# Performance work log

Hardware: AMD Instinct MI355X
Metric: run time of the kernel (lower is better)

The kernel has to match this reference:

```python
import jax, jax.numpy as jnp
import numpy as np

CLS_IDX = 2
DIS_THRESH = 1.0
WEIGHT = 1.0
BIG = 1e9  # sentinel distance for non-boundary lines


def setup_inputs() -> dict:
    key = jax.random.key(0)
    k1, k2, k3, k4 = jax.random.split(key, 4)
    B, T, N, P = 64, 12, 2000, 20
    return {
        "pred_abs": jax.random.normal(k1, (B, T, 2), dtype=jnp.float32),
        "gt_map_pts": jax.random.normal(k2, (B, N, 1, P, 2), dtype=jnp.float32),
        "gt_map_labels": jax.random.randint(k3, (B, N), 0, 4),
        "gt_ego_fut_masks": jax.random.uniform(k4, (B, T), dtype=jnp.float32),
    }


def reference(pred_abs, gt_map_pts, gt_map_labels, gt_ego_fut_masks):
    # pred_abs: [B,T,2]; gt_map_pts: [B,N,1,P,2]; gt_map_labels: [B,N]; masks: [B,T]
    pred_abs = pred_abs.astype(jnp.float32)
    lines = gt_map_pts[:, :, 0].astype(jnp.float32)       # [B,N,P,2]
    valid_line = gt_map_labels == CLS_IDX                  # [B,N]
    has_lines = jnp.any(valid_line, axis=1)                # [B]

    # --- per-timestep min distance to boundary points ---
    diff = pred_abs[:, :, None, None, :] - lines[:, None, :, :, :]   # [B,T,N,P,2]
    dist = jnp.linalg.norm(diff, axis=-1)                            # [B,T,N,P]
    dist = jnp.where(valid_line[:, None, :, None], dist, BIG)
    min_dist = jnp.min(dist, axis=(2, 3))                            # [B,T]
    loss_t = jax.nn.relu(DIS_THRESH - min_dist)                      # [B,T]

    # --- segment intersection: ego step vs boundary segments ---
    origin = jnp.zeros((pred_abs.shape[0], 1, 2), dtype=jnp.float32)
    traj_ext = jnp.concatenate([origin, pred_abs], axis=1)           # [B,T+1,2]
    s1 = traj_ext[:, :-1]                                            # [B,T,2] seg start
    e1 = traj_ext[:, 1:]                                             # [B,T,2] seg end
    bs = lines[:, :, :-1, :]                                         # [B,N,P-1,2]
    be = lines[:, :, 1:, :]                                          # [B,N,P-1,2]

    d1 = e1 - s1                                                     # [B,T,2]
    d2 = be - bs                                                     # [B,N,P-1,2]
    dx1 = d1[..., 0][:, :, None, None]; dy1 = d1[..., 1][:, :, None, None]  # [B,T,1,1]
    dx2 = d2[..., 0][:, None]; dy2 = d2[..., 1][:, None]                    # [B,1,N,P-1]
    det = dx1 * dy2 - dx2 * dy1                                      # [B,T,N,P-1]
    parallel = det == 0
    safe_det = jnp.where(parallel, 1.0, det)
    rel = bs[:, None] - s1[:, :, None, None, :]                      # [B,T,N,P-1,2]
    rx = rel[..., 0]; ry = rel[..., 1]
    t1 = (rx * dy2 - ry * dx2) / safe_det
    t2 = (rx * dy1 - ry * dx1) / safe_det
    intersect = (t1 >= 0) & (t1 <= 1) & (t2 >= 0) & (t2 <= 1) & (~parallel)
    intersect = intersect & valid_line[:, None, :, None]
    crossed = jnp.any(intersect, axis=(2, 3))                        # [B,T]

    # --- early-break semantics: once a valid timestep crosses, drop it and all later t ---
    valid_t = (gt_ego_fut_masks >= 0.5) & has_lines[:, None]          # [B,T]
    trigger = valid_t & crossed
    blocked = jnp.cumsum(trigger.astype(jnp.int32), axis=1) > 0       # inclusive
    include = valid_t & (~blocked)                                    # [B,T]

    total = jnp.sum(jnp.where(include, loss_t, 0.0))
    n_valid = jnp.sum(include.astype(jnp.float32))
    loss = jnp.where(n_valid == 0, 0.0,
                     total / jnp.maximum(n_valid, 1.0) * WEIGHT)
    return jnp.reshape(loss, (1,))


if __name__ == "__main__":
    out = reference(**setup_inputs())
    print(out)
```

## Files before the change

### kernel.cpp

```cpp
#include <hip/hip_runtime.h>

#define BB 64
#define TT 12
#define NL 2000
#define PP 20
#define CLS 2
#define BIGF 1.0e9f

#define LPB   128
#define NBLK  16
#define NSLOT NBLK

#define OFF_CM  (TT * NSLOT * BB)
#define OFF_CNT (TT * NSLOT * BB + NSLOT * BB)

__global__ __launch_bounds__(64) void gtmb_main(
    const float* __restrict__ pred,
    const float* __restrict__ pts,
    const int*   __restrict__ labels,
    unsigned int* __restrict__ ws) {
    const int b    = blockIdx.y;
    const int blk  = blockIdx.x;
    const int lane = threadIdx.x;

    __shared__ unsigned short sidx[LPB];

    const int base = blk * LPB;
    const int n0 = base + 2 * lane;
    int v0 = 0, v1 = 0;
    if (n0 < NL) {
        int2 lb = *reinterpret_cast<const int2*>(labels + b * NL + n0);
        v0 = (lb.x == CLS);
        v1 = (lb.y == CLS);
    }
    unsigned long long m0 = __ballot(v0);
    unsigned long long m1 = __ballot(v1);
    unsigned long long lt = (1ull << lane) - 1ull;
    const int c0  = __popcll(m0);
    const int cnt = c0 + __popcll(m1);
    if (v0) sidx[__popcll(m0 & lt)]      = (unsigned short)n0;
    if (v1) sidx[c0 + __popcll(m1 & lt)] = (unsigned short)(n0 + 1);
    __syncthreads();

    float ex[TT], ey[TT];
    const float* pb = pred + b * (TT * 2);
#pragma unroll
    for (int t = 0; t < TT; ++t) { ex[t] = pb[2*t]; ey[t] = pb[2*t+1]; }

    float mind2[TT];
#pragma unroll
    for (int t = 0; t < TT; ++t) mind2[t] = BIGF;
    unsigned int cmask = 0;

    const int nitems = 2 * cnt;
    for (int w = lane; w < nitems; w += 64) {
        const int ln = sidx[w >> 1];
        const int h  = w & 1;
        const float4* lp = reinterpret_cast<const float4*>(
                               pts + (long)(b * NL + ln) * (PP * 2)) + h * 5;
        float4 q0 = lp[0], q1 = lp[1], q2 = lp[2], q3 = lp[3], q4 = lp[4];
        float p10x = q4.z, p10y = q4.w;
        if (h == 0) { float4 q5 = lp[5]; p10x = q5.x; p10y = q5.y; }

        float px[11], py[11];
        px[0]=q0.x; py[0]=q0.y;  px[1]=q0.z; py[1]=q0.w;
        px[2]=q1.x; py[2]=q1.y;  px[3]=q1.z; py[3]=q1.w;
        px[4]=q2.x; py[4]=q2.y;  px[5]=q2.z; py[5]=q2.w;
        px[6]=q3.x; py[6]=q3.y;  px[7]=q3.z; py[7]=q3.w;
        px[8]=q4.x; py[8]=q4.y;  px[9]=q4.z; py[9]=q4.w;
        px[10]=p10x; py[10]=p10y;

#pragma unroll
        for (int i = 0; i < 10; ++i) {
#pragma unroll
            for (int t = 0; t < TT; ++t) {
                float dx = px[i] - ex[t];
                float dy = py[i] - ey[t];
                mind2[t] = fminf(mind2[t], fmaf(dx, dx, dy * dy));
            }
        }

#pragma unroll
        for (int i = 0; i < 10; ++i) {
            float dx2 = px[i+1] - px[i];
            float dy2 = py[i+1] - py[i];
#pragma unroll
            for (int t = 0; t < TT; ++t) {
                float sx = t ? ex[t-1] : 0.0f;
                float sy = t ? ey[t-1] : 0.0f;
                float dxt = ex[t] - sx;
                float dyt = ey[t] - sy;
                float rx = px[i] - sx;
                float ry = py[i] - sy;
                float det = dxt * dy2 - dx2 * dyt;
                float n1  = rx * dy2 - ry * dx2;
                float n2  = rx * dyt - ry * dxt;
                unsigned int sb = __float_as_uint(det) & 0x80000000u;
                float n1x = __uint_as_float(__float_as_uint(n1) ^ sb);
                float n2x = __uint_as_float(__float_as_uint(n2) ^ sb);
                float ad  = fabsf(det);
                bool hit = (n1x >= 0.0f) & (n1x <= ad) &
                           (n2x >= 0.0f) & (n2x <= ad) & (det != 0.0f);
                if (hit) cmask |= (1u << t);
            }
        }
    }

#pragma unroll
    for (int t = 0; t < TT; ++t) {
        float v = mind2[t];
        for (int off = 32; off; off >>= 1) v = fminf(v, __shfl_xor(v, off));
        mind2[t] = v;
    }
    for (int off = 32; off; off >>= 1) cmask |= __shfl_xor(cmask, off);

    if (lane == 0) {
        float* wf = (float*)ws;
#pragma unroll
        for (int t = 0; t < TT; ++t) wf[(t * NSLOT + blk) * BB + b] = mind2[t];
        ws[OFF_CM  + blk * BB + b] = cmask;
        ws[OFF_CNT + blk * BB + b] = (unsigned int)cnt;
    }
}

__global__ __launch_bounds__(1024) void gtmb_final(
    const float* __restrict__ masks,
    const unsigned int* __restrict__ ws,
    float* __restrict__ out) {
    const int tid = threadIdx.x;
    const int b = tid & 63, g = tid >> 6;

    __shared__ float sm[TT * BB];
    __shared__ unsigned int scm[BB], shas[BB];

    const float* wf = (const float*)ws;
    if (g < TT) {
        float m = BIGF;
#pragma unroll
        for (int s = 0; s < NSLOT; ++s)
            m = fminf(m, wf[(g * NSLOT + s) * BB + b]);
        sm[g * BB + b] = m;
    } else if (g == 12) {
        unsigned int cm = 0;
#pragma unroll
        for (int s = 0; s < NSLOT; ++s) cm |= ws[OFF_CM + s * BB + b];
        scm[b] = cm;
    } else if (g == 13) {
        unsigned int has = 0;
#pragma unroll
        for (int s = 0; s < NSLOT; ++s) has |= ws[OFF_CNT + s * BB + b];
        shas[b] = has;
    }
    __syncthreads();

    if (tid < BB) {
        const bool hl = shas[b] != 0;
        const unsigned int cm = scm[b];
        float total = 0.0f, cnt = 0.0f;
        bool blocked = false;
#pragma unroll
        for (int t = 0; t < TT; ++t) {
            bool valid_t = (masks[b * TT + t] >= 0.5f) && hl;
            bool trig = valid_t && ((cm >> t) & 1u);
            blocked = blocked || trig;
            if (valid_t && !blocked) {
                float d = sqrtf(sm[t * BB + b]);
                total += fmaxf(1.0f - d, 0.0f);
                cnt += 1.0f;
            }
        }
        for (int off = 32; off; off >>= 1) {
            total += __shfl_xor(total, off);
            cnt   += __shfl_xor(cnt, off);
        }
        if (b == 0) out[0] = (cnt == 0.0f) ? 0.0f : total / fmaxf(cnt, 1.0f);
    }
}

extern "C" void kernel_launch(void* const* d_in, const int* in_sizes, int n_in,
                              void* d_out, int out_size, void* d_ws, size_t ws_size,
                              hipStream_t stream) {
    const float* pred   = (const float*)d_in[0];
    const float* pts    = (const float*)d_in[1];
    const int*   labels = (const int*)d_in[2];
    const float* masks  = (const float*)d_in[3];
    float* out = (float*)d_out;
    unsigned int* ws = (unsigned int*)d_ws;

    dim3 grid(NBLK, BB);
    gtmb_main<<<grid, 64, 0, stream>>>(pred, pts, labels, ws);
    gtmb_final<<<1, 1024, 0, stream>>>(masks, ws, out);
}
```

Baseline: 30.52 us.

## Use 512-thread blocks with cross-wave compaction and reduction over fewer line chunks

Each block now covers 500 lines with 8 waves instead of 128 lines with one wave, reducing the grid from 16 to 4 blocks per batch. Valid-line compaction now uses a per-wave count prefix in shared memory, and per-wave minima and crossing masks are combined in shared memory before a single write per block. This cuts the number of partial slots the final kernel reads, at the cost of block-wide barriers and many idle threads, since only about 250 items exist per block.

```diff
diff --git a/kernel.cpp b/kernel.cpp
--- a/kernel.cpp
+++ b/kernel.cpp
@@ -7,28 +7,34 @@
 #define CLS 2
 #define BIGF 1.0e9f
 
-#define LPB   128
-#define NBLK  16
+#define TPB   512
+#define NWAVE 8
+#define LPB   500
+#define NBLK  4
 #define NSLOT NBLK
 
 #define OFF_CM  (TT * NSLOT * BB)
 #define OFF_CNT (TT * NSLOT * BB + NSLOT * BB)
 
-__global__ __launch_bounds__(64) void gtmb_main(
+__global__ __launch_bounds__(TPB) void gtmb_main(
     const float* __restrict__ pred,
     const float* __restrict__ pts,
     const int*   __restrict__ labels,
     unsigned int* __restrict__ ws) {
     const int b    = blockIdx.y;
     const int blk  = blockIdx.x;
-    const int lane = threadIdx.x;
+    const int tid  = threadIdx.x;
+    const int lane = tid & 63, wave = tid >> 6;
 
     __shared__ unsigned short sidx[LPB];
+    __shared__ int wcnt[NWAVE];
+    __shared__ float sred[NWAVE][TT];
+    __shared__ unsigned int scmw[NWAVE];
 
     const int base = blk * LPB;
-    const int n0 = base + 2 * lane;
-    int v0 = 0, v1 = 0;
-    if (n0 < NL) {
+    int v0 = 0, v1 = 0, n0 = 0;
+    if (tid < LPB / 2) {
+        n0 = base + 2 * tid;
         int2 lb = *reinterpret_cast<const int2*>(labels + b * NL + n0);
         v0 = (lb.x == CLS);
         v1 = (lb.y == CLS);
@@ -36,10 +42,18 @@
     unsigned long long m0 = __ballot(v0);
     unsigned long long m1 = __ballot(v1);
     unsigned long long lt = (1ull << lane) - 1ull;
-    const int c0  = __popcll(m0);
-    const int cnt = c0 + __popcll(m1);
-    if (v0) sidx[__popcll(m0 & lt)]      = (unsigned short)n0;
-    if (v1) sidx[c0 + __popcll(m1 & lt)] = (unsigned short)(n0 + 1);
+    if (lane == 0) wcnt[wave] = __popcll(m0) + __popcll(m1);
+    __syncthreads();
+    int off = 0, cnt = 0;
+#pragma unroll
+    for (int w2 = 0; w2 < NWAVE; ++w2) {
+        int c = wcnt[w2];
+        if (w2 < wave) off += c;
+        cnt += c;
+    }
+    const int c0 = __popcll(m0);
+    if (v0) sidx[off + __popcll(m0 & lt)]      = (unsigned short)n0;
+    if (v1) sidx[off + c0 + __popcll(m1 & lt)] = (unsigned short)(n0 + 1);
     __syncthreads();
 
     float ex[TT], ey[TT];
@@ -53,7 +67,7 @@
     unsigned int cmask = 0;
 
     const int nitems = 2 * cnt;
-    for (int w = lane; w < nitems; w += 64) {
+    for (int w = tid; w < nitems; w += TPB) {
         const int ln = sidx[w >> 1];
         const int h  = w & 1;
         const float4* lp = reinterpret_cast<const float4*>(
@@ -109,16 +123,29 @@
 #pragma unroll
     for (int t = 0; t < TT; ++t) {
         float v = mind2[t];
-        for (int off = 32; off; off >>= 1) v = fminf(v, __shfl_xor(v, off));
+        for (int o = 32; o; o >>= 1) v = fminf(v, __shfl_xor(v, o));
         mind2[t] = v;
     }
-    for (int off = 32; off; off >>= 1) cmask |= __shfl_xor(cmask, off);
+    for (int o = 32; o; o >>= 1) cmask |= __shfl_xor(cmask, o);
 
     if (lane == 0) {
-        float* wf = (float*)ws;
-#pragma unroll
-        for (int t = 0; t < TT; ++t) wf[(t * NSLOT + blk) * BB + b] = mind2[t];
-        ws[OFF_CM  + blk * BB + b] = cmask;
+#pragma unroll
+        for (int t = 0; t < TT; ++t) sred[wave][t] = mind2[t];
+        scmw[wave] = cmask;
+    }
+    __syncthreads();
+    float* wf = (float*)ws;
+    if (tid < TT) {
+        float v = sred[0][tid];
+#pragma unroll
+        for (int w2 = 1; w2 < NWAVE; ++w2) v = fminf(v, sred[w2][tid]);
+        wf[(tid * NSLOT + blk) * BB + b] = v;
+    } else if (tid == 16) {
+        unsigned int cm = 0;
+#pragma unroll
+        for (int w2 = 0; w2 < NWAVE; ++w2) cm |= scmw[w2];
+        ws[OFF_CM + blk * BB + b] = cm;
+    } else if (tid == 17) {
         ws[OFF_CNT + blk * BB + b] = (unsigned int)cnt;
     }
 }
@@ -169,9 +196,9 @@
                 cnt += 1.0f;
             }
         }
-        for (int off = 32; off; off >>= 1) {
-            total += __shfl_xor(total, off);
-            cnt   += __shfl_xor(cnt, off);
+        for (int o = 32; o; o >>= 1) {
+            total += __shfl_xor(total, o);
+            cnt   += __shfl_xor(cnt, o);
         }
         if (b == 0) out[0] = (cnt == 0.0f) ? 0.0f : total / fmaxf(cnt, 1.0f);
     }
@@ -188,6 +215,6 @@
     unsigned int* ws = (unsigned int*)d_ws;
 
     dim3 grid(NBLK, BB);
-    gtmb_main<<<grid, 64, 0, stream>>>(pred, pts, labels, ws);
+    gtmb_main<<<grid, TPB, 0, stream>>>(pred, pts, labels, ws);
     gtmb_final<<<1, 1024, 0, stream>>>(masks, ws, out);
 }
```

Result: faster. 27.97 us (-8.4%).
